# Performance work log

Hardware: AMD Instinct MI355X
Metric: run time of the kernel (lower is better)

## Reference

```python
import jax, jax.numpy as jnp
import numpy as np

B, NPG, F, H, DEG = 2048, 50, 64, 2, 8  # graphs, nodes/graph, feat dim, heads, avg degree
N = B * NPG
NEG_SLOPE_ATTN = 0.2   # DGL GATConv default leaky slope
NEG_SLOPE_ACT = 0.1    # module's LeakyReLU


def setup_inputs() -> dict:
    key = jax.random.key(0)
    ks = jax.random.split(key, 24)
    node_feats = jax.random.normal(ks[0], (N, F), dtype=jnp.float32)
    # within-graph random edges + self loops (avoids zero in-degree)
    E = N * DEG
    base = jnp.repeat(jnp.arange(B, dtype=jnp.int32) * NPG, NPG * DEG)
    src = base + jax.random.randint(ks[1], (E,), 0, NPG, dtype=jnp.int32)
    dst = base + jax.random.randint(ks[2], (E,), 0, NPG, dtype=jnp.int32)
    loops = jnp.arange(N, dtype=jnp.int32)
    src = jnp.concatenate([src, loops])
    dst = jnp.concatenate([dst, loops])
    s = 0.1
    params = dict(
        W0=jax.random.normal(ks[3], (F, H * F)) * s,
        al0=jax.random.normal(ks[4], (H, F)) * s,
        ar0=jax.random.normal(ks[5], (H, F)) * s,
        resW0=jax.random.normal(ks[6], (F, H * F)) * s,
        g0=jnp.ones((H * F,)), b0=jnp.zeros((H * F,)),
        W1=jax.random.normal(ks[7], (H * F, H * F)) * s,
        al1=jax.random.normal(ks[8], (H, F)) * s,
        ar1=jax.random.normal(ks[9], (H, F)) * s,
        g1=jnp.ones((H * F,)), b1=jnp.zeros((H * F,)),
        W2=jax.random.normal(ks[10], (H * F, H * F)) * s,
        al2=jax.random.normal(ks[11], (H, F)) * s,
        ar2=jax.random.normal(ks[12], (H, F)) * s,
        g2=jnp.ones((H * F,)), b2=jnp.zeros((H * F,)),
    )
    return {"node_feats": node_feats, **params, "src": src, "dst": dst}


def _gat(h, src, dst, W, al, ar, resW):
    """DGL GATConv (bias=False, residual=True, no activation). resW=None -> identity residual."""
    feat = (h @ W).reshape(N, H, F)                      # [N,H,F]
    el = jnp.sum(feat * al, -1)                          # [N,H]
    er = jnp.sum(feat * ar, -1)
    e = jax.nn.leaky_relu(el[src] + er[dst], NEG_SLOPE_ATTN)  # [E,H]
    m = jax.ops.segment_max(e, dst, num_segments=N)
    ex = jnp.exp(e - m[dst])
    denom = jax.ops.segment_sum(ex, dst, num_segments=N)
    a = ex / denom[dst]                                  # edge softmax per dst node
    rst = jax.ops.segment_sum(a[:, :, None] * feat[src], dst, num_segments=N)
    res = (h @ resW) if resW is not None else h
    return rst + res.reshape(N, H, F)


def _norm(x, g, b):
    mu = jnp.mean(x, -1, keepdims=True)
    v = jnp.mean((x - mu) ** 2, -1, keepdims=True)
    return (x - mu) / jnp.sqrt(v + 1e-5) * g + b


def reference(node_feats, W0, al0, ar0, resW0, g0, b0,
              W1, al1, ar1, g1, b1, W2, al2, ar2, g2, b2, src, dst):
    graph_ids = jnp.arange(N) // NPG
    layers = [(W0, al0, ar0, resW0, g0, b0),
              (W1, al1, ar1, None, g1, b1),
              (W2, al2, ar2, None, g2, b2)]
    h = node_feats
    embeddings = []
    for (W, al, ar, resW, g, b) in layers:
        h = _gat(h, src, dst, W, al, ar, resW).reshape(N, H * F)  # flatten(1)
        h = _norm(h, g, b)
        h = jax.nn.leaky_relu(h, NEG_SLOPE_ACT)
        per_node = h.reshape(N, H, F).mean(1)                     # mean over heads
        emb = jax.ops.segment_sum(per_node, graph_ids, num_segments=B) / NPG  # mean_nodes
        embeddings.append(emb)
    out = jnp.concatenate(embeddings, axis=-1)                    # JK 'cat' -> [B, 3F]
    return jax.nn.leaky_relu(out, NEG_SLOPE_ACT)
```

## Files before the change

kernel.cpp:

```cpp
#include <hip/hip_runtime.h>

#define NPG    50
#define HF     128
#define FDIM   64
#define NGRAPH 2048
#define EPG    400
#define SP     72
#define HB     136
#define CNTW   16

typedef __attribute__((ext_vector_type(8))) short bf16x8;
typedef __attribute__((ext_vector_type(4))) float floatx4;
typedef __bf16 bfv2 __attribute__((ext_vector_type(2)));

__device__ __forceinline__ float leaky(float x, float s) { return x >= 0.f ? x : x * s; }

__device__ __forceinline__ unsigned short f2bf(float f) {
    __bf16 b = (__bf16)f;
    unsigned short u;
    __builtin_memcpy(&u, &b, 2);
    return u;
}
__device__ __forceinline__ unsigned f2bfpk(float a, float b) {
    bfv2 v;
    v[0] = (__bf16)a;
    v[1] = (__bf16)b;
    unsigned u;
    __builtin_memcpy(&u, &v, 4);
    return u;
}
__device__ __forceinline__ float bf2f(unsigned short h) {
    return __uint_as_float(((unsigned)h) << 16);
}
__device__ __forceinline__ int fkey(float f) { int b = __float_as_int(f); return b >= 0 ? b : b ^ 0x7fffffff; }
__device__ __forceinline__ float funkey(int k) { return __int_as_float(k >= 0 ? k : k ^ 0x7fffffff); }

__device__ __forceinline__ void gld16(const void* g, void* l) {
    __builtin_amdgcn_global_load_lds(
        (const __attribute__((address_space(1))) void*)g,
        (__attribute__((address_space(3))) void*)l, 16, 0, 0);
}

__device__ __forceinline__ void stage_wt(const unsigned short* __restrict__ wg,
                                         unsigned short* wtbuf, int t,
                                         int totb, int krsh) {
    const int w = t >> 6, lane = t & 63;
    for (int c = w; c * 1024 < totb; c += 8) {
        int G = c * 1024 + lane * 16;
        int Gs = G ^ (((G >> krsh) & 7) << 4);
        gld16((const char*)wg + Gs, (char*)wtbuf + c * 1024);
    }
}

template <int KROWB>
__device__ __forceinline__ bf16x8 wt_read(const unsigned short* wtbuf, int row, int cb) {
    int byte = (row * KROWB + cb) ^ ((row & 7) << 4);
    return *(const bf16x8*)((const char*)wtbuf + byte);
}

template <int CTRL>
__device__ __forceinline__ float dpp_addx(float x) {
    int yi = __builtin_amdgcn_update_dpp(0, __float_as_int(x), CTRL, 0xf, 0xf, true);
    return x + __int_as_float(yi);
}
__device__ __forceinline__ float row16_sum(float x) {
    x = dpp_addx<0xB1>(x);
    x = dpp_addx<0x4E>(x);
    x = dpp_addx<0x141>(x);
    x = dpp_addx<0x140>(x);
    return x;
}


__global__ void prep_w(const float* __restrict__ W0, const float* __restrict__ rW0,
                       const float* __restrict__ W1, const float* __restrict__ W2,
                       const float* __restrict__ al0, const float* __restrict__ ar0,
                       const float* __restrict__ al1, const float* __restrict__ ar1,
                       const float* __restrict__ al2, const float* __restrict__ ar2,
                       unsigned short* __restrict__ wt0, unsigned short* __restrict__ wt1,
                       unsigned short* __restrict__ wt2) {
    if (blockIdx.x >= 64) {
        int gid = (blockIdx.x - 64) * 256 + threadIdx.x;
        if (gid < 1024) {
            int la = gid >> 6, k = gid & 63;
            unsigned short o = 0;
            if (la < 8) {
                const float* a = (la < 4) ? al0 : ar0;
                int h = (la >> 1) & 1;
                float v = 0.f;
                for (int f = 0; f < 64; ++f) v += W0[k * 128 + h * 64 + f] * a[h * 64 + f];
                __bf16 hi = (__bf16)v;
                if (la & 1) o = f2bf(v - (float)hi);
                else __builtin_memcpy(&o, &hi, 2);
            }
            wt0[(256 + la) * 64 + k] = o;
        } else {
            int q = gid - 1024;
            int l = q >> 11;
            int la = (q >> 7) & 15, kp = q & 127;
            int ktrue = (kp & 64) + ((kp & 3) * 16) + ((kp & 63) >> 2);
            const float* W = l ? W2 : W1;
            unsigned short o = 0;
            if (la < 8) {
                const float* a = l ? ((la < 4) ? al2 : ar2) : ((la < 4) ? al1 : ar1);
                int h = (la >> 1) & 1;
                float v = 0.f;
                for (int f = 0; f < 64; ++f) v += W[ktrue * 128 + h * 64 + f] * a[h * 64 + f];
                __bf16 hi = (__bf16)v;
                if (la & 1) o = f2bf(v - (float)hi);
                else __builtin_memcpy(&o, &hi, 2);
            }
            (l ? wt2 : wt1)[(128 + la) * 128 + kp] = o;
        }
        return;
    }
    int i = blockIdx.x * 256 + threadIdx.x;
    if (i < 256 * 64) {
        int n = i >> 6, k = i & 63;
        float v = (n < 128) ? W0[k * 128 + n] : rW0[k * 128 + (n - 128)];
        wt0[i] = f2bf(v);
    }
    if (i < 128 * 128) {
        int n = i >> 7, kp = i & 127;
        int ktrue = (kp & 64) + ((kp & 3) * 16) + ((kp & 63) >> 2);
        wt1[i] = f2bf(W1[ktrue * 128 + n]);
        wt2[i] = f2bf(W2[ktrue * 128 + n]);
    }
}

template <int K, bool RESW, bool STAGE_NEXT>
__device__ __forceinline__ void gat_layer(
    const float* __restrict__ xrow,
    const unsigned short* __restrict__ wnext,
    const float* __restrict__ gp, const float* __restrict__ bp,
    float* __restrict__ out, int layer, int g, int t,
    unsigned short* wtbuf, unsigned short* featT, unsigned short* hbuf, int* cnt,
    float* el_s, float* er_s, int* elmax_i,
    float* lnp, float* lnq, float* psum4, float* gbL)
{
    const int w = t >> 6, lane = t & 63, quad = lane >> 4, l16 = lane & 15;
    constexpr int KS = K / 32;
    constexpr int KROWB = 2 * K;
    constexpr int ATTN_ROW = RESW ? 256 : 128;
    const int mt = w & 3;
    int mrow = mt * 16 + l16;
    if (mrow >= NPG) mrow = NPG - 1;
    const floatx4 zf = {0.f, 0.f, 0.f, 0.f};

    if (t < HF) {
        int p = (t & 64) + ((t & 15) * 4) + ((t >> 4) & 3);
        gbL[p] = gp[t];
        gbL[HF + p] = bp[t];
    }

    bf16x8 afr[KS];
    if constexpr (RESW) {
        const float* hrow = xrow + (size_t)mrow * 64;
#pragma unroll
        for (int ks = 0; ks < KS; ++ks) {
            int k0 = ks * 32 + quad * 8;
            float4 p0 = *(const float4*)(hrow + k0);
            float4 p1 = *(const float4*)(hrow + k0 + 4);
            unsigned au[4] = {f2bfpk(p0.x, p0.y), f2bfpk(p0.z, p0.w),
                              f2bfpk(p1.x, p1.y), f2bfpk(p1.z, p1.w)};
            __builtin_memcpy(&afr[ks], au, 16);
        }
    } else {
#pragma unroll
        for (int ks = 0; ks < KS; ++ks)
            afr[ks] = *(const bf16x8*)&hbuf[mrow * HB + ks * 32 + quad * 8];
    }

    if constexpr (RESW) {
#pragma unroll 1
        for (int half = 0; half < 2; ++half) {
            const int nb = (w >> 2) * 8 + half * 4;
            floatx4 acc[4];
#pragma unroll
            for (int nt = 0; nt < 4; ++nt) acc[nt] = zf;
#pragma unroll
            for (int nt = 0; nt < 4; ++nt) {
#pragma unroll
                for (int ks = 0; ks < KS; ++ks) {
                    bf16x8 b = wt_read<KROWB>(wtbuf, (nb + nt) * 16 + l16, ks * 64 + quad * 16);
                    acc[nt] = __builtin_amdgcn_mfma_f32_16x16x32_bf16(afr[ks], b, acc[nt], 0, 0, 0);
                }
            }
#pragma unroll
            for (int nt = 0; nt < 4; ++nt) {
                int n = (nb + nt) * 16 + l16;
                if (n < HF) {
                    uint2 pk = {f2bfpk(acc[nt][0], acc[nt][1]),
                                f2bfpk(acc[nt][2], acc[nt][3])};
                    *(uint2*)&featT[n * SP + mt * 16 + quad * 4] = pk;
                } else {
                    int c = n - HF;
                    int spos = (c & 64) + ((c & 15) * 4) + ((c >> 4) & 3);
#pragma unroll
                    for (int r = 0; r < 4; ++r) {
                        int dr = mt * 16 + quad * 4 + r;
                        if (dr < NPG) hbuf[dr * HB + spos] = f2bf(acc[nt][r]);
                    }
                }
            }
        }
    } else {
        const int ntbase = (w >> 2) * 4;
        floatx4 acc[4];
#pragma unroll
        for (int nt = 0; nt < 4; ++nt) acc[nt] = zf;
#pragma unroll
        for (int nt = 0; nt < 4; ++nt) {
#pragma unroll
            for (int ks = 0; ks < KS; ++ks) {
                bf16x8 b = wt_read<KROWB>(wtbuf, (ntbase + nt) * 16 + l16, ks * 64 + quad * 16);
                acc[nt] = __builtin_amdgcn_mfma_f32_16x16x32_bf16(afr[ks], b, acc[nt], 0, 0, 0);
            }
        }
#pragma unroll
        for (int nt = 0; nt < 4; ++nt) {
            int n = (ntbase + nt) * 16 + l16;
            uint2 pk = {f2bfpk(acc[nt][0], acc[nt][1]),
                        f2bfpk(acc[nt][2], acc[nt][3])};
            *(uint2*)&featT[n * SP + mt * 16 + quad * 4] = pk;
        }
    }

    if (w < 4) {
        floatx4 ae = zf;
#pragma unroll
        for (int ks = 0; ks < KS; ++ks) {
            bf16x8 b = wt_read<KROWB>(wtbuf, ATTN_ROW + l16, ks * 64 + quad * 16);
            ae = __builtin_amdgcn_mfma_f32_16x16x32_bf16(afr[ks], b, ae, 0, 0, 0);
        }
#pragma unroll
        for (int r = 0; r < 4; ++r) {
            float v = dpp_addx<0xB1>(ae[r]);
            if ((l16 & 1) == 0 && l16 < 8) {
                int row = mt * 16 + quad * 4 + r;
                int hd2 = (l16 >> 1) & 1;
                if (l16 < 4) {
                    el_s[hd2 * 64 + row] = v;
                    atomicMax(&elmax_i[hd2], fkey(v));
                } else {
                    er_s[hd2 * 64 + row] = v;
                }
            }
        }
    }
    __syncthreads();

    if constexpr (STAGE_NEXT) stage_wt(wnext, wtbuf, t, 144 * 256, 8);

    const int hd = w >> 2, amt = w & 3;
    const int d = amt * 16 + l16;

    const float erd = er_s[hd * 64 + d];
    const float md = leaky(funkey(elmax_i[hd]) + erd, 0.2f);
    const int dcl = d < NPG ? d : NPG - 1;
    const int* crow = &cnt[dcl * CNTW];

    bf16x8 ap[2];
    float rowsum = 0.f;
#pragma unroll
    for (int ks = 0; ks < 2; ++ks) {
        float4 ev0 = *(const float4*)&el_s[hd * 64 + ks * 32 + quad * 8];
        float4 ev1 = *(const float4*)&el_s[hd * 64 + ks * 32 + quad * 8 + 4];
        const float ev[8] = {ev0.x, ev0.y, ev0.z, ev0.w, ev1.x, ev1.y, ev1.z, ev1.w};
        int2 cw = *(const int2*)&crow[ks * 8 + quad * 2];
        unsigned au[4];
#pragma unroll
        for (int jp = 0; jp < 4; ++jp) {
            float e0 = ev[2 * jp] + erd;
            float e1 = ev[2 * jp + 1] + erd;
            e0 = fmaxf(e0, 0.2f * e0);
            e1 = fmaxf(e1, 0.2f * e1);
            float p0 = __expf(e0 - md);
            float p1 = __expf(e1 - md);
            int w32 = (jp & 2) ? cw.y : cw.x;
            int sh = (jp & 1) * 16;
            int c0 = (w32 >> sh) & 0xff;
            int c1 = (w32 >> (sh + 8)) & 0xff;
            unsigned pk = f2bfpk((float)c0 * p0, (float)c1 * p1);
            au[jp] = pk;
            rowsum += __uint_as_float(pk << 16) + __uint_as_float(pk & 0xffff0000u);
        }
        __builtin_memcpy(&ap[ks], au, 16);
    }
    rowsum += __shfl_xor(rowsum, 16, 64);
    rowsum += __shfl_xor(rowsum, 32, 64);
    const float rden = 1.f / fmaxf(rowsum, 1e-30f);

    floatx4 ag[4];
#pragma unroll
    for (int nt = 0; nt < 4; ++nt) ag[nt] = zf;
#pragma unroll
    for (int nt = 0; nt < 4; ++nt) {
        const unsigned short* fr = &featT[(hd * 64 + nt * 16 + l16) * SP];
#pragma unroll
        for (int ks = 0; ks < 2; ++ks) {
            bf16x8 b = *(const bf16x8*)(fr + ks * 32 + quad * 8);
            ag[nt] = __builtin_amdgcn_mfma_f32_16x16x32_bf16(ap[ks], b, ag[nt], 0, 0, 0);
        }
    }

    float s1[4] = {0, 0, 0, 0}, s2[4] = {0, 0, 0, 0};
#pragma unroll
    for (int r = 0; r < 4; ++r) {
        int dd = amt * 16 + quad * 4 + r;
        int dc = dd < NPG ? dd : NPG - 1;
        float rdv = __shfl(rden, quad * 4 + r, 16);
        uint2 rv = *(const uint2*)&hbuf[dc * HB + hd * 64 + l16 * 4];
#pragma unroll
        for (int nt = 0; nt < 4; ++nt) {
            unsigned hw = (nt & 1) ? ((nt & 2) ? rv.y >> 16 : rv.x >> 16)
                                   : ((nt & 2) ? rv.y & 0xffffu : rv.x & 0xffffu);
            float vv = fmaf(ag[nt][r], rdv, bf2f((unsigned short)hw));
            ag[nt][r] = vv;
            s1[r] += vv;
            s2[r] = fmaf(vv, vv, s2[r]);
        }
    }
#pragma unroll
    for (int r = 0; r < 4; ++r) {
        s1[r] = row16_sum(s1[r]);
        s2[r] = row16_sum(s2[r]);
    }
    if (l16 == 0) {
#pragma unroll
        for (int r = 0; r < 4; ++r) {
            int dd = amt * 16 + quad * 4 + r;
            lnp[hd * 64 + dd] = s1[r];
            lnq[hd * 64 + dd] = s2[r];
        }
    }
    __syncthreads();

    if (t < 2) elmax_i[t] = (int)0x80000000;

    float4 ga = *(const float4*)&gbL[hd * 64 + l16 * 4];
    float4 ba = *(const float4*)&gbL[HF + hd * 64 + l16 * 4];

    float part[4] = {0, 0, 0, 0};
#pragma unroll
    for (int r = 0; r < 4; ++r) {
        int dd = amt * 16 + quad * 4 + r;
        if (dd < NPG) {
            float mu = (lnp[dd] + lnp[64 + dd]) * (1.f / HF);
            float rs = rsqrtf((lnq[dd] + lnq[64 + dd]) * (1.f / HF) - mu * mu + 1e-5f);
            float y4[4];
#pragma unroll
            for (int nt = 0; nt < 4; ++nt) {
                float y = (ag[nt][r] - mu) * rs * ga[nt] + ba[nt];
                y = leaky(y, 0.1f);
                y4[nt] = y;
                part[nt] += y;
            }
            uint2 pk = {f2bfpk(y4[0], y4[1]), f2bfpk(y4[2], y4[3])};
            *(uint2*)&hbuf[dd * HB + hd * 64 + l16 * 4] = pk;
        }
    }
#pragma unroll
    for (int nt = 0; nt < 4; ++nt) {
        part[nt] += __shfl_xor(part[nt], 16, 64);
        part[nt] += __shfl_xor(part[nt], 32, 64);
    }
    if (quad == 0) {
#pragma unroll
        for (int nt = 0; nt < 4; ++nt)
            psum4[amt * HF + hd * 64 + nt * 16 + l16] = part[nt];
    }
    __syncthreads();

    if (t < FDIM) {
        float s = 0.f;
#pragma unroll
        for (int a4 = 0; a4 < 4; ++a4)
            s += psum4[a4 * HF + t] + psum4[a4 * HF + t + FDIM];
        out[(size_t)g * (3 * FDIM) + layer * FDIM + t] = leaky(s * (1.f / (2 * NPG)), 0.1f);
    }
}

__global__ __launch_bounds__(512, 4) void gat3_kernel(
    const float* __restrict__ x,
    const unsigned short* __restrict__ wt0,
    const unsigned short* __restrict__ wt1,
    const unsigned short* __restrict__ wt2,
    const float* __restrict__ g0, const float* __restrict__ b0,
    const float* __restrict__ g1, const float* __restrict__ b1,
    const float* __restrict__ g2, const float* __restrict__ b2,
    const int* __restrict__ src, const int* __restrict__ dst,
    float* __restrict__ out)
{
    __shared__ unsigned short wtbuf[144 * 128];
    __shared__ unsigned short featT[HF * SP];
    __shared__ unsigned short hbuf[NPG * HB];
    __shared__ int cnt[NPG * CNTW];
    __shared__ float el_s[128], er_s[128];
    __shared__ int elmax_i[2];
    __shared__ float lnp[128], lnq[128];
    __shared__ float psum4[4 * HF];
    __shared__ float gbL[2 * HF];

    const int g = blockIdx.x, t = threadIdx.x;
    const int nbase = g * NPG;

    stage_wt(wt0, wtbuf, t, 272 * 128, 7);

    int es = 0, ed = 0;
    if (t < EPG) { es = src[g * EPG + t] - nbase; ed = dst[g * EPG + t] - nbase; }

    for (int i = t; i < NPG * CNTW; i += 512) cnt[i] = 0;
    if (t < 2) elmax_i[t] = (int)0x80000000;
    __syncthreads();

    if (t < EPG) atomicAdd(&cnt[ed * CNTW + (es >> 2)], 1 << ((es & 3) * 8));
    if (t < NPG) atomicAdd(&cnt[t * CNTW + (t >> 2)], 1 << ((t & 3) * 8));

    const float* xrow = x + (size_t)nbase * 64;
    gat_layer<64, true, true>(xrow, wt1, g0, b0, out, 0, g, t,
                              wtbuf, featT, hbuf, cnt, el_s, er_s, elmax_i, lnp, lnq, psum4, gbL);
    gat_layer<128, false, true>(nullptr, wt2, g1, b1, out, 1, g, t,
                                wtbuf, featT, hbuf, cnt, el_s, er_s, elmax_i, lnp, lnq, psum4, gbL);
    gat_layer<128, false, false>(nullptr, nullptr, g2, b2, out, 2, g, t,
                                 wtbuf, featT, hbuf, cnt, el_s, er_s, elmax_i, lnp, lnq, psum4, gbL);
}

extern "C" void kernel_launch(void* const* d_in, const int* in_sizes, int n_in,
                              void* d_out, int out_size, void* d_ws, size_t ws_size,
                              hipStream_t stream) {
    const float* x   = (const float*)d_in[0];
    const float* W0  = (const float*)d_in[1];
    const float* al0 = (const float*)d_in[2];
    const float* ar0 = (const float*)d_in[3];
    const float* rW0 = (const float*)d_in[4];
    const float* g0  = (const float*)d_in[5];
    const float* b0  = (const float*)d_in[6];
    const float* W1  = (const float*)d_in[7];
    const float* al1 = (const float*)d_in[8];
    const float* ar1 = (const float*)d_in[9];
    const float* g1  = (const float*)d_in[10];
    const float* b1  = (const float*)d_in[11];
    const float* W2  = (const float*)d_in[12];
    const float* al2 = (const float*)d_in[13];
    const float* ar2 = (const float*)d_in[14];
    const float* g2  = (const float*)d_in[15];
    const float* b2  = (const float*)d_in[16];
    const int* src   = (const int*)d_in[17];
    const int* dst   = (const int*)d_in[18];
    float* out = (float*)d_out;

    unsigned short* wt0 = (unsigned short*)d_ws;
    unsigned short* wt1 = wt0 + 272 * 64;
    unsigned short* wt2 = wt1 + 144 * 128;

    prep_w<<<84, 256, 0, stream>>>(W0, rW0, W1, W2, al0, ar0, al1, ar1, al2, ar2,
                                   wt0, wt1, wt2);
    gat3_kernel<<<NGRAPH, 512, 0, stream>>>(
        x, wt0, wt1, wt2, g0, b0, g1, b1, g2, b2, src, dst, out);
}
```

Before: 182.9 us.

## Shrink shared memory to raise occupancy by splitting weight staging across buffers

Replaces the separate shared arrays with one packed byte buffer of about 54KB, so that more 512-thread blocks can fit per CU; launch bounds are raised from 4 to 6. Next-layer weights are now staged in two halves, one into the weight region and one into the feature region after it is consumed. This needs an extra barrier, and the layer-0 GEMM holds all 8 accumulator tiles at once instead of processing them in two passes. Adjacency counts are packed as 4-bit nibbles and the partial sums are stored as bf16. Both changes cut LDS footprint but risk count overflow and some loss of precision.

```diff
diff --git a/kernel.cpp b/kernel.cpp
--- a/kernel.cpp
+++ b/kernel.cpp
@@ -5,9 +5,18 @@
 #define FDIM   64
 #define NGRAPH 2048
 #define EPG    400
-#define SP     72
-#define HB     136
-#define CNTW   16
+
+#define WT_OFF  0
+#define FT_OFF  18432
+#define HB_OFF  36864
+#define CNT_OFF 49664
+#define ELS_OFF 51264
+#define ERS_OFF 51776
+#define EMX_OFF 52288
+#define LNP_OFF 52304
+#define LNQ_OFF 52816
+#define PSM_OFF 53328
+#define SMEM_SZ 54352
 
 typedef __attribute__((ext_vector_type(8))) short bf16x8;
 typedef __attribute__((ext_vector_type(4))) float floatx4;
@@ -41,21 +50,28 @@
         (__attribute__((address_space(3))) void*)l, 16, 0, 0);
 }
 
-__device__ __forceinline__ void stage_wt(const unsigned short* __restrict__ wg,
-                                         unsigned short* wtbuf, int t,
-                                         int totb, int krsh) {
+__device__ __forceinline__ void stage_full(const unsigned short* __restrict__ wg,
+                                           unsigned char* smem, int t, int chunks) {
     const int w = t >> 6, lane = t & 63;
-    for (int c = w; c * 1024 < totb; c += 8) {
-        int G = c * 1024 + lane * 16;
-        int Gs = G ^ (((G >> krsh) & 7) << 4);
-        gld16((const char*)wg + Gs, (char*)wtbuf + c * 1024);
-    }
-}
-
-template <int KROWB>
-__device__ __forceinline__ bf16x8 wt_read(const unsigned short* wtbuf, int row, int cb) {
-    int byte = (row * KROWB + cb) ^ ((row & 7) << 4);
-    return *(const bf16x8*)((const char*)wtbuf + byte);
+    for (int c = w; c < chunks; c += 8) {
+        int D = c * 1024 + lane * 16;
+        int P = D ^ (((D >> 7) & 7) << 4);
+        gld16((const char*)wg + P, smem + c * 1024);
+    }
+}
+__device__ __forceinline__ void stage_half(const unsigned short* __restrict__ wg,
+                                           unsigned char* dst, int t, int h) {
+    const int w = t >> 6, lane = t & 63;
+    for (int c = w; c < 18; c += 8) {
+        int D = c * 1024 + lane * 16;
+        int P = D ^ (((D >> 7) & 7) << 4);
+        int row = P >> 7, colb = P & 127;
+        gld16((const char*)wg + row * 256 + h * 128 + colb, dst + c * 1024);
+    }
+}
+__device__ __forceinline__ bf16x8 rd128(const unsigned char* base, int row, int cb) {
+    int sw = (row * 128 + cb) ^ ((row & 7) << 4);
+    return *(const bf16x8*)(base + sw);
 }
 
 template <int CTRL>
@@ -70,7 +86,6 @@
     x = dpp_addx<0x140>(x);
     return x;
 }
-
 
 __global__ void prep_w(const float* __restrict__ W0, const float* __restrict__ rW0,
                        const float* __restrict__ W1, const float* __restrict__ W2,
@@ -134,24 +149,24 @@
     const unsigned short* __restrict__ wnext,
     const float* __restrict__ gp, const float* __restrict__ bp,
     float* __restrict__ out, int layer, int g, int t,
-    unsigned short* wtbuf, unsigned short* featT, unsigned short* hbuf, int* cnt,
-    float* el_s, float* er_s, int* elmax_i,
-    float* lnp, float* lnq, float* psum4, float* gbL)
+    unsigned char* smem)
 {
     const int w = t >> 6, lane = t & 63, quad = lane >> 4, l16 = lane & 15;
     constexpr int KS = K / 32;
-    constexpr int KROWB = 2 * K;
-    constexpr int ATTN_ROW = RESW ? 256 : 128;
     const int mt = w & 3;
     int mrow = mt * 16 + l16;
     if (mrow >= NPG) mrow = NPG - 1;
     const floatx4 zf = {0.f, 0.f, 0.f, 0.f};
 
-    if (t < HF) {
-        int p = (t & 64) + ((t & 15) * 4) + ((t >> 4) & 3);
-        gbL[p] = gp[t];
-        gbL[HF + p] = bp[t];
-    }
+    unsigned char* FT = smem + FT_OFF;
+    unsigned char* HBp = smem + HB_OFF;
+    const int* cnt = (const int*)(smem + CNT_OFF);
+    float* el_s = (float*)(smem + ELS_OFF);
+    float* er_s = (float*)(smem + ERS_OFF);
+    int* elmax_i = (int*)(smem + EMX_OFF);
+    float* lnp = (float*)(smem + LNP_OFF);
+    float* lnq = (float*)(smem + LNQ_OFF);
+    unsigned short* psm = (unsigned short*)(smem + PSM_OFF);
 
     bf16x8 afr[KS];
     if constexpr (RESW) {
@@ -167,70 +182,39 @@
         }
     } else {
 #pragma unroll
-        for (int ks = 0; ks < KS; ++ks)
-            afr[ks] = *(const bf16x8*)&hbuf[mrow * HB + ks * 32 + quad * 8];
-    }
-
-    if constexpr (RESW) {
-#pragma unroll 1
-        for (int half = 0; half < 2; ++half) {
-            const int nb = (w >> 2) * 8 + half * 4;
-            floatx4 acc[4];
-#pragma unroll
-            for (int nt = 0; nt < 4; ++nt) acc[nt] = zf;
-#pragma unroll
-            for (int nt = 0; nt < 4; ++nt) {
-#pragma unroll
-                for (int ks = 0; ks < KS; ++ks) {
-                    bf16x8 b = wt_read<KROWB>(wtbuf, (nb + nt) * 16 + l16, ks * 64 + quad * 16);
-                    acc[nt] = __builtin_amdgcn_mfma_f32_16x16x32_bf16(afr[ks], b, acc[nt], 0, 0, 0);
-                }
-            }
-#pragma unroll
-            for (int nt = 0; nt < 4; ++nt) {
-                int n = (nb + nt) * 16 + l16;
-                if (n < HF) {
-                    uint2 pk = {f2bfpk(acc[nt][0], acc[nt][1]),
-                                f2bfpk(acc[nt][2], acc[nt][3])};
-                    *(uint2*)&featT[n * SP + mt * 16 + quad * 4] = pk;
-                } else {
-                    int c = n - HF;
-                    int spos = (c & 64) + ((c & 15) * 4) + ((c >> 4) & 3);
-#pragma unroll
-                    for (int r = 0; r < 4; ++r) {
-                        int dr = mt * 16 + quad * 4 + r;
-                        if (dr < NPG) hbuf[dr * HB + spos] = f2bf(acc[nt][r]);
-                    }
-                }
-            }
-        }
-    } else {
-        const int ntbase = (w >> 2) * 4;
-        floatx4 acc[4];
-#pragma unroll
-        for (int nt = 0; nt < 4; ++nt) acc[nt] = zf;
-#pragma unroll
-        for (int nt = 0; nt < 4; ++nt) {
-#pragma unroll
-            for (int ks = 0; ks < KS; ++ks) {
-                bf16x8 b = wt_read<KROWB>(wtbuf, (ntbase + nt) * 16 + l16, ks * 64 + quad * 16);
-                acc[nt] = __builtin_amdgcn_mfma_f32_16x16x32_bf16(afr[ks], b, acc[nt], 0, 0, 0);
-            }
-        }
-#pragma unroll
-        for (int nt = 0; nt < 4; ++nt) {
-            int n = (ntbase + nt) * 16 + l16;
-            uint2 pk = {f2bfpk(acc[nt][0], acc[nt][1]),
-                        f2bfpk(acc[nt][2], acc[nt][3])};
-            *(uint2*)&featT[n * SP + mt * 16 + quad * 4] = pk;
+        for (int ks = 0; ks < KS; ++ks) {
+            int byte = (mrow * 256 + ks * 64 + quad * 16) ^ ((mrow & 7) << 4);
+            afr[ks] = *(const bf16x8*)(HBp + byte);
+        }
+    }
+
+    floatx4 acc[RESW ? 8 : 4];
+    constexpr int NT = RESW ? 8 : 4;
+#pragma unroll
+    for (int nt = 0; nt < NT; ++nt) acc[nt] = zf;
+#pragma unroll
+    for (int nt = 0; nt < NT; ++nt) {
+        int rowb = ((w >> 2) * NT + nt) * 16 + l16;
+#pragma unroll
+        for (int ks = 0; ks < KS; ++ks) {
+            bf16x8 b;
+            if constexpr (RESW) {
+                b = rd128(smem, rowb, ks * 64 + quad * 16);
+            } else {
+                b = rd128(ks < 2 ? smem : FT, rowb, (ks & 1) * 64 + quad * 16);
+            }
+            acc[nt] = __builtin_amdgcn_mfma_f32_16x16x32_bf16(afr[ks], b, acc[nt], 0, 0, 0);
         }
     }
 
     if (w < 4) {
+        constexpr int AROW = RESW ? 256 : 128;
         floatx4 ae = zf;
 #pragma unroll
         for (int ks = 0; ks < KS; ++ks) {
-            bf16x8 b = wt_read<KROWB>(wtbuf, ATTN_ROW + l16, ks * 64 + quad * 16);
+            bf16x8 b;
+            if constexpr (RESW) b = rd128(smem, AROW + l16, ks * 64 + quad * 16);
+            else b = rd128(ks < 2 ? smem : FT, AROW + l16, (ks & 1) * 64 + quad * 16);
             ae = __builtin_amdgcn_mfma_f32_16x16x32_bf16(afr[ks], b, ae, 0, 0, 0);
         }
 #pragma unroll
@@ -250,7 +234,30 @@
     }
     __syncthreads();
 
-    if constexpr (STAGE_NEXT) stage_wt(wnext, wtbuf, t, 144 * 256, 8);
+    if constexpr (STAGE_NEXT) stage_half(wnext, smem + WT_OFF, t, 0);
+
+#pragma unroll
+    for (int nt = 0; nt < NT; ++nt) {
+        int n = ((w >> 2) * NT + nt) * 16 + l16;
+        if (n < HF) {
+            uint2 pk = {f2bfpk(acc[nt][0], acc[nt][1]),
+                        f2bfpk(acc[nt][2], acc[nt][3])};
+            int fb = (n * 128 + mt * 32 + quad * 8) ^ ((n & 7) << 4);
+            *(uint2*)(FT + fb) = pk;
+        } else {
+            int c = n - HF;
+            int spos = (c & 64) + ((c & 15) * 4) + ((c >> 4) & 3);
+#pragma unroll
+            for (int r = 0; r < 4; ++r) {
+                int dr = mt * 16 + quad * 4 + r;
+                if (dr < NPG) {
+                    int byte = (dr * 256 + spos * 2) ^ ((dr & 7) << 4);
+                    *(unsigned short*)(HBp + byte) = f2bf(acc[nt][r]);
+                }
+            }
+        }
+    }
+    __syncthreads();
 
     const int hd = w >> 2, amt = w & 3;
     const int d = amt * 16 + l16;
@@ -258,7 +265,7 @@
     const float erd = er_s[hd * 64 + d];
     const float md = leaky(funkey(elmax_i[hd]) + erd, 0.2f);
     const int dcl = d < NPG ? d : NPG - 1;
-    const int* crow = &cnt[dcl * CNTW];
+    const int* crow = cnt + dcl * 8;
 
     bf16x8 ap[2];
     float rowsum = 0.f;
@@ -267,7 +274,7 @@
         float4 ev0 = *(const float4*)&el_s[hd * 64 + ks * 32 + quad * 8];
         float4 ev1 = *(const float4*)&el_s[hd * 64 + ks * 32 + quad * 8 + 4];
         const float ev[8] = {ev0.x, ev0.y, ev0.z, ev0.w, ev1.x, ev1.y, ev1.z, ev1.w};
-        int2 cw = *(const int2*)&crow[ks * 8 + quad * 2];
+        int w32 = crow[ks * 4 + quad];
         unsigned au[4];
 #pragma unroll
         for (int jp = 0; jp < 4; ++jp) {
@@ -277,10 +284,8 @@
             e1 = fmaxf(e1, 0.2f * e1);
             float p0 = __expf(e0 - md);
             float p1 = __expf(e1 - md);
-            int w32 = (jp & 2) ? cw.y : cw.x;
-            int sh = (jp & 1) * 16;
-            int c0 = (w32 >> sh) & 0xff;
-            int c1 = (w32 >> (sh + 8)) & 0xff;
+            int c0 = (w32 >> (8 * jp)) & 15;
+            int c1 = (w32 >> (8 * jp + 4)) & 15;
             unsigned pk = f2bfpk((float)c0 * p0, (float)c1 * p1);
             au[jp] = pk;
             rowsum += __uint_as_float(pk << 16) + __uint_as_float(pk & 0xffff0000u);
@@ -296,10 +301,9 @@
     for (int nt = 0; nt < 4; ++nt) ag[nt] = zf;
 #pragma unroll
     for (int nt = 0; nt < 4; ++nt) {
-        const unsigned short* fr = &featT[(hd * 64 + nt * 16 + l16) * SP];
 #pragma unroll
         for (int ks = 0; ks < 2; ++ks) {
-            bf16x8 b = *(const bf16x8*)(fr + ks * 32 + quad * 8);
+            bf16x8 b = rd128(FT, hd * 64 + nt * 16 + l16, ks * 64 + quad * 16);
             ag[nt] = __builtin_amdgcn_mfma_f32_16x16x32_bf16(ap[ks], b, ag[nt], 0, 0, 0);
         }
     }
@@ -310,7 +314,8 @@
         int dd = amt * 16 + quad * 4 + r;
         int dc = dd < NPG ? dd : NPG - 1;
         float rdv = __shfl(rden, quad * 4 + r, 16);
-        uint2 rv = *(const uint2*)&hbuf[dc * HB + hd * 64 + l16 * 4];
+        int byte = (dc * 256 + hd * 128 + l16 * 8) ^ ((dc & 7) << 4);
+        uint2 rv = *(const uint2*)(HBp + byte);
 #pragma unroll
         for (int nt = 0; nt < 4; ++nt) {
             unsigned hw = (nt & 1) ? ((nt & 2) ? rv.y >> 16 : rv.x >> 16)
@@ -336,10 +341,16 @@
     }
     __syncthreads();
 
+    if constexpr (STAGE_NEXT) stage_half(wnext, FT, t, 1);
+
     if (t < 2) elmax_i[t] = (int)0x80000000;
 
-    float4 ga = *(const float4*)&gbL[hd * 64 + l16 * 4];
-    float4 ba = *(const float4*)&gbL[HF + hd * 64 + l16 * 4];
+    float ga_[4], ba_[4];
+#pragma unroll
+    for (int nt = 0; nt < 4; ++nt) {
+        ga_[nt] = gp[hd * 64 + nt * 16 + l16];
+        ba_[nt] = bp[hd * 64 + nt * 16 + l16];
+    }
 
     float part[4] = {0, 0, 0, 0};
 #pragma unroll
@@ -351,13 +362,14 @@
             float y4[4];
 #pragma unroll
             for (int nt = 0; nt < 4; ++nt) {
-                float y = (ag[nt][r] - mu) * rs * ga[nt] + ba[nt];
+                float y = (ag[nt][r] - mu) * rs * ga_[nt] + ba_[nt];
                 y = leaky(y, 0.1f);
                 y4[nt] = y;
                 part[nt] += y;
             }
             uint2 pk = {f2bfpk(y4[0], y4[1]), f2bfpk(y4[2], y4[3])};
-            *(uint2*)&hbuf[dd * HB + hd * 64 + l16 * 4] = pk;
+            int byte = (dd * 256 + hd * 128 + l16 * 8) ^ ((dd & 7) << 4);
+            *(uint2*)(HBp + byte) = pk;
         }
     }
 #pragma unroll
@@ -368,7 +380,7 @@
     if (quad == 0) {
 #pragma unroll
         for (int nt = 0; nt < 4; ++nt)
-            psum4[amt * HF + hd * 64 + nt * 16 + l16] = part[nt];
+            psm[amt * HF + hd * 64 + nt * 16 + l16] = f2bf(part[nt]);
     }
     __syncthreads();
 
@@ -376,12 +388,12 @@
         float s = 0.f;
 #pragma unroll
         for (int a4 = 0; a4 < 4; ++a4)
-            s += psum4[a4 * HF + t] + psum4[a4 * HF + t + FDIM];
+            s += bf2f(psm[a4 * HF + t]) + bf2f(psm[a4 * HF + t + FDIM]);
         out[(size_t)g * (3 * FDIM) + layer * FDIM + t] = leaky(s * (1.f / (2 * NPG)), 0.1f);
     }
 }
 
-__global__ __launch_bounds__(512, 4) void gat3_kernel(
+__global__ __launch_bounds__(512, 6) void gat3_kernel(
     const float* __restrict__ x,
     const unsigned short* __restrict__ wt0,
     const unsigned short* __restrict__ wt1,
@@ -392,38 +404,29 @@
     const int* __restrict__ src, const int* __restrict__ dst,
     float* __restrict__ out)
 {
-    __shared__ unsigned short wtbuf[144 * 128];
-    __shared__ unsigned short featT[HF * SP];
-    __shared__ unsigned short hbuf[NPG * HB];
-    __shared__ int cnt[NPG * CNTW];
-    __shared__ float el_s[128], er_s[128];
-    __shared__ int elmax_i[2];
-    __shared__ float lnp[128], lnq[128];
-    __shared__ float psum4[4 * HF];
-    __shared__ float gbL[2 * HF];
+    __shared__ __align__(16) unsigned char smem[SMEM_SZ];
 
     const int g = blockIdx.x, t = threadIdx.x;
     const int nbase = g * NPG;
-
-    stage_wt(wt0, wtbuf, t, 272 * 128, 7);
+    int* cnt = (int*)(smem + CNT_OFF);
+    int* elmax_i = (int*)(smem + EMX_OFF);
+
+    stage_full(wt0, smem, t, 34);
 
     int es = 0, ed = 0;
     if (t < EPG) { es = src[g * EPG + t] - nbase; ed = dst[g * EPG + t] - nbase; }
 
-    for (int i = t; i < NPG * CNTW; i += 512) cnt[i] = 0;
+    if (t < 400) cnt[t] = 0;
     if (t < 2) elmax_i[t] = (int)0x80000000;
     __syncthreads();
 
-    if (t < EPG) atomicAdd(&cnt[ed * CNTW + (es >> 2)], 1 << ((es & 3) * 8));
-    if (t < NPG) atomicAdd(&cnt[t * CNTW + (t >> 2)], 1 << ((t & 3) * 8));
+    if (t < EPG) atomicAdd(&cnt[ed * 8 + (es >> 3)], 1 << ((es & 7) * 4));
+    if (t < NPG) atomicAdd(&cnt[t * 8 + (t >> 3)], 1 << ((t & 7) * 4));
 
     const float* xrow = x + (size_t)nbase * 64;
-    gat_layer<64, true, true>(xrow, wt1, g0, b0, out, 0, g, t,
-                              wtbuf, featT, hbuf, cnt, el_s, er_s, elmax_i, lnp, lnq, psum4, gbL);
-    gat_layer<128, false, true>(nullptr, wt2, g1, b1, out, 1, g, t,
-                                wtbuf, featT, hbuf, cnt, el_s, er_s, elmax_i, lnp, lnq, psum4, gbL);
-    gat_layer<128, false, false>(nullptr, nullptr, g2, b2, out, 2, g, t,
-                                 wtbuf, featT, hbuf, cnt, el_s, er_s, elmax_i, lnp, lnq, psum4, gbL);
+    gat_layer<64, true, true>(xrow, wt1, g0, b0, out, 0, g, t, smem);
+    gat_layer<128, false, true>(nullptr, wt2, g1, b1, out, 1, g, t, smem);
+    gat_layer<128, false, false>(nullptr, nullptr, g2, b2, out, 2, g, t, smem);
 }
 
 extern "C" void kernel_launch(void* const* d_in, const int* in_sizes, int n_in,
```

Result: slower. 226.9 us (+24.1%).
